# Performance work log

Measured on AMD Instinct MI355X. Metric: run time of the kernel, lower is better.

Reference implementation:

```python
import jax, jax.numpy as jnp
import numpy as np

D_MODEL = 1024
NUM_HEADS = 16
HEAD_DIM = D_MODEL // NUM_HEADS


def setup_inputs() -> dict:
    key = jax.random.key(0)
    ks = jax.random.split(key, 9)
    B, S = 2, 2048
    scale = 1.0 / np.sqrt(D_MODEL)
    inp = {
        "x": jax.random.normal(ks[0], (B, S, D_MODEL), dtype=jnp.float32),
        "Wq": jax.random.normal(ks[1], (D_MODEL, D_MODEL), dtype=jnp.float32) * scale,
        "bq": jnp.zeros((D_MODEL,), dtype=jnp.float32),
        "Wk": jax.random.normal(ks[2], (D_MODEL, D_MODEL), dtype=jnp.float32) * scale,
        "bk": jnp.zeros((D_MODEL,), dtype=jnp.float32),
        "Wv": jax.random.normal(ks[3], (D_MODEL, D_MODEL), dtype=jnp.float32) * scale,
        "bv": jnp.zeros((D_MODEL,), dtype=jnp.float32),
        "Wo": jax.random.normal(ks[4], (D_MODEL, D_MODEL), dtype=jnp.float32) * scale,
        "bo": jnpp_zeros(D_MODEL) if False else jnp.zeros((D_MODEL,), dtype=jnp.float32),
    }
    return inp


def reference(x, Wq, bq, Wk, bk, Wv, bv, Wo, bo):
    B, S, _ = x.shape
    # projections (torch Linear: y = x @ W.T + b; here W stored as [in, out])
    q = x @ Wq + bq  # [B,S,D]
    k = x @ Wk + bk
    v = x @ Wv + bv
    # split heads -> [B,H,S,hd]
    def split(t):
        return t.reshape(B, S, NUM_HEADS, HEAD_DIM).transpose(0, 2, 1, 3)
    q, k, v = split(q), split(k), split(v)
    scale = 1.0 / jnp.sqrt(jnp.asarray(HEAD_DIM, dtype=x.dtype))
    scores = jnp.einsum("bhqd,bhkd->bhqk", q, k) * scale  # [B,H,S,S]
    probs = jax.nn.softmax(scores, axis=-1)
    out = jnp.einsum("bhqk,bhkd->bhqd", probs, v)  # [B,H,S,hd]
    out = out.transpose(0, 2, 1, 3).reshape(B, S, D_MODEL)
    return out @ Wo + bo  # dropout is identity in eval mode
```

## Files before the change

kernel.cpp:

```cpp
#include <hip/hip_runtime.h>

#define D_MODEL 1024
#define NHEADS  16
#define HDIM    64
#define BATCH   2
#define SEQ     2048
#define M_TOK   (BATCH * SEQ)

typedef unsigned short u16;
typedef unsigned int   u32;
typedef __attribute__((ext_vector_type(8))) short  short8;
typedef __attribute__((ext_vector_type(4))) float  floatx4;
typedef __attribute__((ext_vector_type(2))) u32    u32x2;

#define GLOBAL_AS __attribute__((address_space(1)))
#define LDS_AS    __attribute__((address_space(3)))

static __device__ __forceinline__ void gload_lds16(const u16* g, u16* l) {
    __builtin_amdgcn_global_load_lds((const GLOBAL_AS u32*)g, (LDS_AS u32*)l, 16, 0, 0);
}

static __device__ __forceinline__ u16 f2bf(float f) {
    union { float f; u32 i; } v; v.f = f;
    u32 x = v.i;
    return (u16)((x + 0x7fffu + ((x >> 16) & 1u)) >> 16);
}

static __device__ __forceinline__ u32 cvtpk(float a, float b) {
    u32 r;
    asm("v_cvt_pk_bf16_f32 %0, %1, %2" : "=v"(r) : "v"(a), "v"(b));
    return r;
}

static __device__ __forceinline__ short8 ld8_cvt(const float* __restrict__ p) {
    float4 f0 = *(const float4*)(p);
    float4 f1 = *(const float4*)(p + 4);
    short8 r;
    r[0] = (short)f2bf(f0.x); r[1] = (short)f2bf(f0.y);
    r[2] = (short)f2bf(f0.z); r[3] = (short)f2bf(f0.w);
    r[4] = (short)f2bf(f1.x); r[5] = (short)f2bf(f1.y);
    r[6] = (short)f2bf(f1.z); r[7] = (short)f2bf(f1.w);
    return r;
}

__global__ __launch_bounds__(256) void zerofill_k(float* __restrict__ out, int n) {
    int i = blockIdx.x * 256 + threadIdx.x;
    if (i < n) out[i] = 0.f;
}

__global__ __launch_bounds__(1024) void prep_k(const float* __restrict__ x,
                                               const float* __restrict__ W0,
                                               const float* __restrict__ W1,
                                               const float* __restrict__ W2,
                                               const float* __restrict__ W3,
                                               u16* __restrict__ WtBase,
                                               u16* __restrict__ Xb) {
    int z = blockIdx.z;
    if (z == 4) {
        int blk = blockIdx.y * 32 + blockIdx.x;
        int t   = threadIdx.y * 32 + threadIdx.x;
        size_t i0 = ((size_t)blk * 1024 + t) * 4;
        float4 f = *(const float4*)(x + i0);
        u32 lo = (u32)f2bf(f.x) | ((u32)f2bf(f.y) << 16);
        u32 hi = (u32)f2bf(f.z) | ((u32)f2bf(f.w) << 16);
        *(u32*)(Xb + i0)     = lo;
        *(u32*)(Xb + i0 + 2) = hi;
        return;
    }
    const float* W = (z == 0) ? W0 : (z == 1) ? W1 : (z == 2) ? W2 : W3;
    u16* Wt = WtBase + (size_t)z * 1024 * 1024;
    __shared__ u16 tile[32][33];
    int tx = threadIdx.x, ty = threadIdx.y;
    int bx = blockIdx.x * 32, by = blockIdx.y * 32;
    tile[ty][tx] = f2bf(W[(size_t)(by + ty) * 1024 + bx + tx]);
    __syncthreads();
    Wt[(size_t)(bx + ty) * 1024 + by + tx] = tile[tx][ty];
}

template <int MODE, int OUTF32, int MI>
static __device__ __forceinline__ void gemm_core(u16* __restrict__ smem,
                                                 const u16* __restrict__ A,
                                                 const u16* __restrict__ Bt,
                                                 const float* __restrict__ bias,
                                                 float scale,
                                                 void* __restrict__ C,
                                                 int m0, int n0) {
    u16* As = smem;
    u16* Bs = smem + MI * 32 * 32;
    int tid  = threadIdx.x;
    int wave = tid >> 6, lane = tid & 63;
    int quad = lane >> 4, l15 = lane & 15;
    int wm = (wave & 1) * (MI * 16);
    int wn = (wave >> 1) * 64;

    floatx4 acc[MI][4] = {};

    for (int k0 = 0; k0 < 1024; k0 += 32) {
#pragma unroll
        for (int t = 0; t < MI / 2; ++t) {
            int a = t * 256 + tid;
            gload_lds16(A + (size_t)(m0 + (a >> 2)) * 1024 + k0 + (a & 3) * 8, As + (size_t)a * 8);
        }
#pragma unroll
        for (int t = 0; t < 2; ++t) {
            int cb = t * 256 + tid;
            gload_lds16(Bt + (size_t)(n0 + (cb >> 2)) * 1024 + k0 + (cb & 3) * 8, Bs + (size_t)cb * 8);
        }
        __syncthreads();

        short8 af[MI], bfr[4];
#pragma unroll
        for (int i = 0; i < MI; ++i)
            af[i] = *(const short8*)(As + (wm + i * 16 + l15) * 32 + quad * 8);
#pragma unroll
        for (int j = 0; j < 4; ++j)
            bfr[j] = *(const short8*)(Bs + (wn + j * 16 + l15) * 32 + quad * 8);
#pragma unroll
        for (int i = 0; i < MI; ++i)
#pragma unroll
            for (int j = 0; j < 4; ++j)
                acc[i][j] = __builtin_amdgcn_mfma_f32_16x16x32_bf16(af[i], bfr[j], acc[i][j], 0, 0, 0);
        __syncthreads();
    }

    if constexpr (MODE == 2) {
        u16* T = smem;
        int bb = m0 >> 11;
#pragma unroll
        for (int p = 0; p < 2; ++p) {
            if (p) __syncthreads();
            if ((wave >> 1) == p) {
#pragma unroll
                for (int j = 0; j < 4; ++j) {
                    int dcol = j * 16 + l15;
                    float bv = bias[n0 + p * 64 + dcol];
#pragma unroll
                    for (int i = 0; i < MI; ++i) {
#pragma unroll
                        for (int rr = 0; rr < 2; ++rr) {
                            int srow = wm + i * 16 + quad * 4 + rr * 2;
                            u16 lo = f2bf((acc[i][j][rr * 2]     + bv) * scale);
                            u16 hi = f2bf((acc[i][j][rr * 2 + 1] + bv) * scale);
                            *(u32*)(T + dcol * 136 + srow) = (u32)lo | ((u32)hi << 16);
                        }
                    }
                }
            }
            __syncthreads();
            int d  = tid >> 2;
            int sc = (tid & 3) * 32;
            int col = n0 + p * 64 + d;
            int h = col >> 6, dd = col & 63;
            int s0 = (m0 & 2047) + sc;
            size_t gbase = (((size_t)bb * NHEADS + h) * HDIM + dd) * SEQ + s0;
#pragma unroll
            for (int c = 0; c < 4; ++c)
                *(short8*)((u16*)C + gbase + c * 8) = *(const short8*)(T + d * 136 + sc + c * 8);
        }
        return;
    }

#pragma unroll
    for (int j = 0; j < 4; ++j) {
        int col = n0 + wn + j * 16 + l15;
        float bv = bias[col];
#pragma unroll
        for (int i = 0; i < MI; ++i) {
#pragma unroll
            for (int r = 0; r < 4; ++r) {
                int row = m0 + wm + i * 16 + quad * 4 + r;
                float v = (acc[i][j][r] + bv) * scale;
                size_t idx;
                if (MODE == 0) {
                    idx = (size_t)row * 1024 + col;
                } else {
                    int b = row >> 11, s = row & 2047;
                    int h = col >> 6,  d = col & 63;
                    idx = (((size_t)b * NHEADS + h) * SEQ + s) * HDIM + d;
                }
                if constexpr (OUTF32) ((float*)C)[idx] = v;
                else                  ((u16*)C)[idx] = f2bf(v);
            }
        }
    }
}

__global__ __launch_bounds__(256, 3) void gemm_qkv(const u16* __restrict__ X,
                                                   const u16* __restrict__ WtBase,
                                                   const float* __restrict__ bq,
                                                   const float* __restrict__ bk,
                                                   const float* __restrict__ bv,
                                                   u16* __restrict__ OutBase) {
    __shared__ __align__(16) u16 smem[8704];
    int z = blockIdx.z;
    const u16* Bt     = WtBase + (size_t)z * 1024 * 1024;
    const float* bias = (z == 0) ? bq : (z == 1) ? bk : bv;
    u16* C            = OutBase + (size_t)z * (size_t)M_TOK * 1024;
    if (z == 2)
        gemm_core<2, 0, 4>(smem, X, Bt, bias, 1.0f, C, blockIdx.y * 128, blockIdx.x * 128);
    else if (z == 0)
        gemm_core<1, 0, 4>(smem, X, Bt, bias, 0.18033688011112042f , C,
                           blockIdx.y * 128, blockIdx.x * 128);
    else
        gemm_core<1, 0, 4>(smem, X, Bt, bias, 1.0f, C, blockIdx.y * 128, blockIdx.x * 128);
}

__global__ __launch_bounds__(256, 2) void gemm_out(const u16* __restrict__ A,
                                                   const u16* __restrict__ Bt,
                                                   const float* __restrict__ bias,
                                                   float* __restrict__ C) {
    __shared__ __align__(16) u16 smem[6144];
    gemm_core<0, 1, 2>(smem, A, Bt, bias, 1.0f, C, blockIdx.y * 64, blockIdx.x * 128);
}

#define PST2 40
__global__ __launch_bounds__(512, 3) void attn_k(const u16* __restrict__ Q,
                                                 const u16* __restrict__ K,
                                                 const u16* __restrict__ Vt_g,
                                                 u16* __restrict__ O) {
    __shared__ __align__(16) u16 Vt[2][64 * 128];
    __shared__ __align__(16) u16 Kt[2][128 * 64];
    __shared__ __align__(16) u16 Pl[8][16 * PST2];

    int tid  = threadIdx.x;
    int wave = tid >> 6, lane = tid & 63;
    int quad = lane >> 4, l15 = lane & 15;
    int bh = blockIdx.y;
    int b = bh >> 4, h = bh & 15;
    const u16* Qb = Q    + (size_t)bh * SEQ * HDIM;
    const u16* Kb = K    + (size_t)bh * SEQ * HDIM;
    const u16* Vb = Vt_g + (size_t)bh * HDIM * SEQ;
    int q0 = blockIdx.x * 128 + wave * 16;

    short8 qf0 = *(const short8*)(Qb + (size_t)(q0 + l15) * 64 + quad * 8);
    short8 qf1 = *(const short8*)(Qb + (size_t)(q0 + l15) * 64 + 32 + quad * 8);

    short8 onesf;
#pragma unroll
    for (int i = 0; i < 8; ++i) onesf[i] = (short)0x3F80;

    floatx4 o[4] = {};
    floatx4 o_sum = {};

    {
#pragma unroll
        for (int rnd = 0; rnd < 2; ++rnd) {
            int g = rnd * 512 + tid;
            int vrow = g >> 4, vc = g & 15;
            gload_lds16(Vb + (size_t)vrow * SEQ + (vc ^ (vrow & 15)) * 8,
                        Vt[0] + (size_t)g * 8);
            int krow = g >> 3, kc = g & 7;
            gload_lds16(Kb + (size_t)krow * 64 + (kc ^ (krow & 7)) * 8,
                        Kt[0] + (size_t)g * 8);
        }
    }

    for (int it = 0; it < SEQ / 128; ++it) {
        int kv0 = it * 128;
        __syncthreads();

        if (it + 1 < SEQ / 128) {
            u16* vdst = Vt[(it + 1) & 1];
            u16* kdst = Kt[(it + 1) & 1];
#pragma unroll
            for (int rnd = 0; rnd < 2; ++rnd) {
                int g = rnd * 512 + tid;
                int vrow = g >> 4, vc = g & 15;
                gload_lds16(Vb + (size_t)vrow * SEQ + kv0 + 128 + (vc ^ (vrow & 15)) * 8,
                            vdst + (size_t)g * 8);
                int krow = g >> 3, kc = g & 7;
                gload_lds16(Kb + (size_t)(kv0 + 128 + krow) * 64 + (kc ^ (krow & 7)) * 8,
                            kdst + (size_t)g * 8);
            }
        }

        const u16* kb = Kt[it & 1];
        floatx4 s[8];
        __builtin_amdgcn_s_setprio(1);
#pragma unroll
        for (int j = 0; j < 8; ++j) {
            int row = j * 16 + l15;
            const u16* kr = kb + (size_t)row * 64;
            short8 k0 = *(const short8*)(kr + ((quad ^ (l15 & 7)) * 8));
            short8 k1 = *(const short8*)(kr + (((quad + 4) ^ (l15 & 7)) * 8));
            floatx4 a = {};
            a = __builtin_amdgcn_mfma_f32_16x16x32_bf16(k0, qf0, a, 0, 0, 0);
            a = __builtin_amdgcn_mfma_f32_16x16x32_bf16(k1, qf1, a, 0, 0, 0);
            s[j] = a;
        }
        __builtin_amdgcn_s_setprio(0);

        const u16* vb = Vt[it & 1];
#pragma unroll
        for (int kh = 0; kh < 4; ++kh) {
#pragma unroll
            for (int t = 0; t < 2; ++t) {
                int j = kh * 2 + t;
                float p0 = exp2f(s[j][0]), p1 = exp2f(s[j][1]);
                float p2 = exp2f(s[j][2]), p3 = exp2f(s[j][3]);
                u32 w0 = cvtpk(p0, p1), w1 = cvtpk(p2, p3);
                *(u32x2*)(&Pl[wave][l15 * PST2 + t * 16 + quad * 4]) = (u32x2){w0, w1};
            }
            short8 pf = *(const short8*)(&Pl[wave][l15 * PST2 + quad * 8]);
            __builtin_amdgcn_s_setprio(1);
#pragma unroll
            for (int dj = 0; dj < 4; ++dj) {
                int row = dj * 16 + l15;
                int cg  = kh * 4 + quad;
                short8 vf = *(const short8*)(&vb[(row * 16 + (cg ^ l15)) * 8]);
                o[dj] = __builtin_amdgcn_mfma_f32_16x16x32_bf16(pf, vf, o[dj], 0, 0, 0);
            }
            o_sum = __builtin_amdgcn_mfma_f32_16x16x32_bf16(pf, onesf, o_sum, 0, 0, 0);
            __builtin_amdgcn_s_setprio(0);
        }
    }

#pragma unroll
    for (int r = 0; r < 4; ++r) {
        float invq = 1.f / o_sum[r];
        int srow = q0 + quad * 4 + r;
        size_t base = ((size_t)b * SEQ + srow) * D_MODEL + h * HDIM;
#pragma unroll
        for (int dj = 0; dj < 4; ++dj)
            O[base + dj * 16 + l15] = f2bf(o[dj][r] * invq);
    }
}

extern "C" void kernel_launch(void* const* d_in, const int* in_sizes, int n_in,
                              void* d_out, int out_size, void* d_ws, size_t ws_size,
                              hipStream_t stream) {
    const float* x  = (const float*)d_in[0];
    const float* Wq = (const float*)d_in[1];
    const float* bq = (const float*)d_in[2];
    const float* Wk = (const float*)d_in[3];
    const float* bk = (const float*)d_in[4];
    const float* Wv = (const float*)d_in[5];
    const float* bv = (const float*)d_in[6];
    const float* Wo = (const float*)d_in[7];
    const float* bo = (const float*)d_in[8];
    float* out = (float*)d_out;

    char* ws = (char*)d_ws;
    const size_t WSZ = (size_t)1024 * 1024 * sizeof(u16);
    const size_t QSZ = (size_t)M_TOK * 1024 * sizeof(u16);
    const size_t NEED = 4 * WSZ + 4 * QSZ;

    if (ws_size < NEED) {
        zerofill_k<<<dim3((out_size + 255) / 256), 256, 0, stream>>>(out, out_size);
        return;
    }

    u16* wtq = (u16*)(ws);
    u16* wto = (u16*)(ws + 3 * WSZ);
    u16* Qw  = (u16*)(ws + 4 * WSZ);
    u16* Kw  = (u16*)(ws + 4 * WSZ + QSZ);
    u16* Vw  = (u16*)(ws + 4 * WSZ + 2 * QSZ);
    u16* Xb  = (u16*)(ws + 4 * WSZ + 3 * QSZ);
    u16* Aw  = Xb;

    prep_k<<<dim3(32, 32, 5), dim3(32, 32), 0, stream>>>(x, Wq, Wk, Wv, Wo, wtq, Xb);

    gemm_qkv<<<dim3(8, 32, 3), 256, 0, stream>>>(Xb, wtq, bq, bk, bv, Qw);
    attn_k<<<dim3(SEQ / 128, BATCH * NHEADS), 512, 0, stream>>>(Qw, Kw, Vw, Aw);
    gemm_out<<<dim3(8, 64), 256, 0, stream>>>(Aw, wto, bo, out);
}
```

Before: 203.1 us.

## Shrink attention tiles to 64 queries/64 keys and vectorize prep kernel

The attention kernel moves from 512-thread blocks with 128-query, 128-key tiles to 256-thread blocks with 64-query, 64-key tiles. It adjusts the LDS swizzle for the narrower V tile and doubles the grid, aiming for more resident blocks and less LDS per block. The trade-off is that each K/V tile is now reused by fewer query rows, so global traffic and barrier count go up. The prep kernel now uses 256 threads with vectorized float loads and 16-byte bf16 stores for both the x conversion and the weight transpose.

```diff
diff --git a/kernel.cpp b/kernel.cpp
--- a/kernel.cpp
+++ b/kernel.cpp
@@ -48,33 +48,44 @@
     if (i < n) out[i] = 0.f;
 }
 
-__global__ __launch_bounds__(1024) void prep_k(const float* __restrict__ x,
-                                               const float* __restrict__ W0,
-                                               const float* __restrict__ W1,
-                                               const float* __restrict__ W2,
-                                               const float* __restrict__ W3,
-                                               u16* __restrict__ WtBase,
-                                               u16* __restrict__ Xb) {
+__global__ __launch_bounds__(256) void prep_k(const float* __restrict__ x,
+                                              const float* __restrict__ W0,
+                                              const float* __restrict__ W1,
+                                              const float* __restrict__ W2,
+                                              const float* __restrict__ W3,
+                                              u16* __restrict__ WtBase,
+                                              u16* __restrict__ Xb) {
     int z = blockIdx.z;
+    int t = threadIdx.x;
     if (z == 4) {
         int blk = blockIdx.y * 32 + blockIdx.x;
-        int t   = threadIdx.y * 32 + threadIdx.x;
-        size_t i0 = ((size_t)blk * 1024 + t) * 4;
-        float4 f = *(const float4*)(x + i0);
+        size_t i0 = ((size_t)blk * 256 + t) * 16;
+        short8 v0 = ld8_cvt(x + i0);
+        short8 v1 = ld8_cvt(x + i0 + 8);
+        *(short8*)(Xb + i0)     = v0;
+        *(short8*)(Xb + i0 + 8) = v1;
+        return;
+    }
+    const float* W = (z == 0) ? W0 : (z == 1) ? W1 : (z == 2) ? W2 : W3;
+    u16* Wt = WtBase + (size_t)z * 1024 * 1024;
+    __shared__ u16 T[32][34];
+    int bx = blockIdx.x * 32, by = blockIdx.y * 32;
+    {
+        int r = t >> 3, c4 = t & 7;
+        float4 f = *(const float4*)(W + (size_t)(by + r) * 1024 + bx + c4 * 4);
         u32 lo = (u32)f2bf(f.x) | ((u32)f2bf(f.y) << 16);
         u32 hi = (u32)f2bf(f.z) | ((u32)f2bf(f.w) << 16);
-        *(u32*)(Xb + i0)     = lo;
-        *(u32*)(Xb + i0 + 2) = hi;
-        return;
-    }
-    const float* W = (z == 0) ? W0 : (z == 1) ? W1 : (z == 2) ? W2 : W3;
-    u16* Wt = WtBase + (size_t)z * 1024 * 1024;
-    __shared__ u16 tile[32][33];
-    int tx = threadIdx.x, ty = threadIdx.y;
-    int bx = blockIdx.x * 32, by = blockIdx.y * 32;
-    tile[ty][tx] = f2bf(W[(size_t)(by + ty) * 1024 + bx + tx]);
+        *(u32*)(&T[r][c4 * 4])     = lo;
+        *(u32*)(&T[r][c4 * 4 + 2]) = hi;
+    }
     __syncthreads();
-    Wt[(size_t)(bx + ty) * 1024 + by + tx] = tile[tx][ty];
+    if (t < 128) {
+        int n = t >> 2, seg = t & 3;
+        short8 v;
+#pragma unroll
+        for (int i = 0; i < 8; ++i) v[i] = (short)T[seg * 8 + i][n];
+        *(short8*)(Wt + (size_t)(bx + n) * 1024 + by + seg * 8) = v;
+    }
 }
 
 template <int MODE, int OUTF32, int MI>
@@ -214,13 +225,13 @@
 }
 
 #define PST2 40
-__global__ __launch_bounds__(512, 3) void attn_k(const u16* __restrict__ Q,
+__global__ __launch_bounds__(256, 4) void attn_k(const u16* __restrict__ Q,
                                                  const u16* __restrict__ K,
                                                  const u16* __restrict__ Vt_g,
                                                  u16* __restrict__ O) {
-    __shared__ __align__(16) u16 Vt[2][64 * 128];
-    __shared__ __align__(16) u16 Kt[2][128 * 64];
-    __shared__ __align__(16) u16 Pl[8][16 * PST2];
+    __shared__ __align__(16) u16 Vt[2][64 * 64];
+    __shared__ __align__(16) u16 Kt[2][64 * 64];
+    __shared__ __align__(16) u16 Pl[4][16 * PST2];
 
     int tid  = threadIdx.x;
     int wave = tid >> 6, lane = tid & 63;
@@ -230,7 +241,7 @@
     const u16* Qb = Q    + (size_t)bh * SEQ * HDIM;
     const u16* Kb = K    + (size_t)bh * SEQ * HDIM;
     const u16* Vb = Vt_g + (size_t)bh * HDIM * SEQ;
-    int q0 = blockIdx.x * 128 + wave * 16;
+    int q0 = blockIdx.x * 64 + wave * 16;
 
     short8 qf0 = *(const short8*)(Qb + (size_t)(q0 + l15) * 64 + quad * 8);
     short8 qf1 = *(const short8*)(Qb + (size_t)(q0 + l15) * 64 + 32 + quad * 8);
@@ -245,40 +256,38 @@
     {
 #pragma unroll
         for (int rnd = 0; rnd < 2; ++rnd) {
-            int g = rnd * 512 + tid;
-            int vrow = g >> 4, vc = g & 15;
-            gload_lds16(Vb + (size_t)vrow * SEQ + (vc ^ (vrow & 15)) * 8,
+            int g = rnd * 256 + tid;
+            int row = g >> 3, c = g & 7;
+            gload_lds16(Vb + (size_t)row * SEQ + (c ^ (row & 7)) * 8,
                         Vt[0] + (size_t)g * 8);
-            int krow = g >> 3, kc = g & 7;
-            gload_lds16(Kb + (size_t)krow * 64 + (kc ^ (krow & 7)) * 8,
+            gload_lds16(Kb + (size_t)row * 64 + (c ^ (row & 7)) * 8,
                         Kt[0] + (size_t)g * 8);
         }
     }
 
-    for (int it = 0; it < SEQ / 128; ++it) {
-        int kv0 = it * 128;
+    for (int it = 0; it < SEQ / 64; ++it) {
+        int kv0 = it * 64;
         __syncthreads();
 
-        if (it + 1 < SEQ / 128) {
+        if (it + 1 < SEQ / 64) {
             u16* vdst = Vt[(it + 1) & 1];
             u16* kdst = Kt[(it + 1) & 1];
 #pragma unroll
             for (int rnd = 0; rnd < 2; ++rnd) {
-                int g = rnd * 512 + tid;
-                int vrow = g >> 4, vc = g & 15;
-                gload_lds16(Vb + (size_t)vrow * SEQ + kv0 + 128 + (vc ^ (vrow & 15)) * 8,
+                int g = rnd * 256 + tid;
+                int row = g >> 3, c = g & 7;
+                gload_lds16(Vb + (size_t)row * SEQ + kv0 + 64 + (c ^ (row & 7)) * 8,
                             vdst + (size_t)g * 8);
-                int krow = g >> 3, kc = g & 7;
-                gload_lds16(Kb + (size_t)(kv0 + 128 + krow) * 64 + (kc ^ (krow & 7)) * 8,
+                gload_lds16(Kb + (size_t)(kv0 + 64 + row) * 64 + (c ^ (row & 7)) * 8,
                             kdst + (size_t)g * 8);
             }
         }
 
         const u16* kb = Kt[it & 1];
-        floatx4 s[8];
+        floatx4 s[4];
         __builtin_amdgcn_s_setprio(1);
 #pragma unroll
-        for (int j = 0; j < 8; ++j) {
+        for (int j = 0; j < 4; ++j) {
             int row = j * 16 + l15;
             const u16* kr = kb + (size_t)row * 64;
             short8 k0 = *(const short8*)(kr + ((quad ^ (l15 & 7)) * 8));
@@ -292,7 +301,7 @@
 
         const u16* vb = Vt[it & 1];
 #pragma unroll
-        for (int kh = 0; kh < 4; ++kh) {
+        for (int kh = 0; kh < 2; ++kh) {
 #pragma unroll
             for (int t = 0; t < 2; ++t) {
                 int j = kh * 2 + t;
@@ -305,9 +314,9 @@
             __builtin_amdgcn_s_setprio(1);
 #pragma unroll
             for (int dj = 0; dj < 4; ++dj) {
-                int row = dj * 16 + l15;
-                int cg  = kh * 4 + quad;
-                short8 vf = *(const short8*)(&vb[(row * 16 + (cg ^ l15)) * 8]);
+                int drow = dj * 16 + l15;
+                short8 vf = *(const short8*)(&vb[((size_t)drow * 8 +
+                                                  ((kh * 4 + quad) ^ (l15 & 7))) * 8]);
                 o[dj] = __builtin_amdgcn_mfma_f32_16x16x32_bf16(pf, vf, o[dj], 0, 0, 0);
             }
             o_sum = __builtin_amdgcn_mfma_f32_16x16x32_bf16(pf, onesf, o_sum, 0, 0, 0);
@@ -358,9 +367,9 @@
     u16* Xb  = (u16*)(ws + 4 * WSZ + 3 * QSZ);
     u16* Aw  = Xb;
 
-    prep_k<<<dim3(32, 32, 5), dim3(32, 32), 0, stream>>>(x, Wq, Wk, Wv, Wo, wtq, Xb);
+    prep_k<<<dim3(32, 32, 5), 256, 0, stream>>>(x, Wq, Wk, Wv, Wo, wtq, Xb);
 
     gemm_qkv<<<dim3(8, 32, 3), 256, 0, stream>>>(Xb, wtq, bq, bk, bv, Qw);
-    attn_k<<<dim3(SEQ / 128, BATCH * NHEADS), 512, 0, stream>>>(Qw, Kw, Vw, Aw);
+    attn_k<<<dim3(SEQ / 64, BATCH * NHEADS), 256, 0, stream>>>(Qw, Kw, Vw, Aw);
     gemm_out<<<dim3(8, 64), 256, 0, stream>>>(Aw, wto, bo, out);
 }
```

Result: no change. 205.3 us (+1.1%).

## Double GEMM K-tile to 64 with XOR-swizzled LDS and vectorize prep kernel

Applied to the files above, without the earlier changes.

The GEMM core now stages 64-wide K slices per iteration instead of 32. This halves the number of barrier pairs per tile, and an XOR swizzle on the LDS layout avoids bank conflicts on the 128-byte rows. The prep kernel is rewritten to 256 threads using float4 loads and 16-byte stores, for both the x conversion and the weight transpose. LDS per block doubles, which may reduce occupancy for gemm_qkv under its launch bound of 3.

```diff
diff --git a/kernel.cpp b/kernel.cpp
--- a/kernel.cpp
+++ b/kernel.cpp
@@ -48,33 +48,44 @@
     if (i < n) out[i] = 0.f;
 }
 
-__global__ __launch_bounds__(1024) void prep_k(const float* __restrict__ x,
-                                               const float* __restrict__ W0,
-                                               const float* __restrict__ W1,
-                                               const float* __restrict__ W2,
-                                               const float* __restrict__ W3,
-                                               u16* __restrict__ WtBase,
-                                               u16* __restrict__ Xb) {
+__global__ __launch_bounds__(256) void prep_k(const float* __restrict__ x,
+                                              const float* __restrict__ W0,
+                                              const float* __restrict__ W1,
+                                              const float* __restrict__ W2,
+                                              const float* __restrict__ W3,
+                                              u16* __restrict__ WtBase,
+                                              u16* __restrict__ Xb) {
     int z = blockIdx.z;
+    int t = threadIdx.x;
     if (z == 4) {
         int blk = blockIdx.y * 32 + blockIdx.x;
-        int t   = threadIdx.y * 32 + threadIdx.x;
-        size_t i0 = ((size_t)blk * 1024 + t) * 4;
-        float4 f = *(const float4*)(x + i0);
+        size_t i0 = ((size_t)blk * 256 + t) * 16;
+        short8 v0 = ld8_cvt(x + i0);
+        short8 v1 = ld8_cvt(x + i0 + 8);
+        *(short8*)(Xb + i0)     = v0;
+        *(short8*)(Xb + i0 + 8) = v1;
+        return;
+    }
+    const float* W = (z == 0) ? W0 : (z == 1) ? W1 : (z == 2) ? W2 : W3;
+    u16* Wt = WtBase + (size_t)z * 1024 * 1024;
+    __shared__ u16 T[32][34];
+    int bx = blockIdx.x * 32, by = blockIdx.y * 32;
+    {
+        int r = t >> 3, c4 = t & 7;
+        float4 f = *(const float4*)(W + (size_t)(by + r) * 1024 + bx + c4 * 4);
         u32 lo = (u32)f2bf(f.x) | ((u32)f2bf(f.y) << 16);
         u32 hi = (u32)f2bf(f.z) | ((u32)f2bf(f.w) << 16);
-        *(u32*)(Xb + i0)     = lo;
-        *(u32*)(Xb + i0 + 2) = hi;
-        return;
-    }
-    const float* W = (z == 0) ? W0 : (z == 1) ? W1 : (z == 2) ? W2 : W3;
-    u16* Wt = WtBase + (size_t)z * 1024 * 1024;
-    __shared__ u16 tile[32][33];
-    int tx = threadIdx.x, ty = threadIdx.y;
-    int bx = blockIdx.x * 32, by = blockIdx.y * 32;
-    tile[ty][tx] = f2bf(W[(size_t)(by + ty) * 1024 + bx + tx]);
+        *(u32*)(&T[r][c4 * 4])     = lo;
+        *(u32*)(&T[r][c4 * 4 + 2]) = hi;
+    }
     __syncthreads();
-    Wt[(size_t)(bx + ty) * 1024 + by + tx] = tile[tx][ty];
+    if (t < 128) {
+        int n = t >> 2, seg = t & 3;
+        short8 v;
+#pragma unroll
+        for (int i = 0; i < 8; ++i) v[i] = (short)T[seg * 8 + i][n];
+        *(short8*)(Wt + (size_t)(bx + n) * 1024 + by + seg * 8) = v;
+    }
 }
 
 template <int MODE, int OUTF32, int MI>
@@ -86,7 +97,7 @@
                                                  void* __restrict__ C,
                                                  int m0, int n0) {
     u16* As = smem;
-    u16* Bs = smem + MI * 32 * 32;
+    u16* Bs = smem + MI * 32 * 64;
     int tid  = threadIdx.x;
     int wave = tid >> 6, lane = tid & 63;
     int quad = lane >> 4, l15 = lane & 15;
@@ -95,31 +106,39 @@
 
     floatx4 acc[MI][4] = {};
 
-    for (int k0 = 0; k0 < 1024; k0 += 32) {
-#pragma unroll
-        for (int t = 0; t < MI / 2; ++t) {
+    for (int k0 = 0; k0 < 1024; k0 += 64) {
+#pragma unroll
+        for (int t = 0; t < MI; ++t) {
             int a = t * 256 + tid;
-            gload_lds16(A + (size_t)(m0 + (a >> 2)) * 1024 + k0 + (a & 3) * 8, As + (size_t)a * 8);
-        }
-#pragma unroll
-        for (int t = 0; t < 2; ++t) {
-            int cb = t * 256 + tid;
-            gload_lds16(Bt + (size_t)(n0 + (cb >> 2)) * 1024 + k0 + (cb & 3) * 8, Bs + (size_t)cb * 8);
+            int row = a >> 3, c = a & 7;
+            gload_lds16(A + (size_t)(m0 + row) * 1024 + k0 + ((c ^ (row & 7)) * 8),
+                        As + (size_t)a * 8);
+        }
+#pragma unroll
+        for (int t = 0; t < 4; ++t) {
+            int a = t * 256 + tid;
+            int row = a >> 3, c = a & 7;
+            gload_lds16(Bt + (size_t)(n0 + row) * 1024 + k0 + ((c ^ (row & 7)) * 8),
+                        Bs + (size_t)a * 8);
         }
         __syncthreads();
 
-        short8 af[MI], bfr[4];
-#pragma unroll
-        for (int i = 0; i < MI; ++i)
-            af[i] = *(const short8*)(As + (wm + i * 16 + l15) * 32 + quad * 8);
-#pragma unroll
-        for (int j = 0; j < 4; ++j)
-            bfr[j] = *(const short8*)(Bs + (wn + j * 16 + l15) * 32 + quad * 8);
-#pragma unroll
-        for (int i = 0; i < MI; ++i)
+#pragma unroll
+        for (int h = 0; h < 2; ++h) {
+            int g = ((h * 4 + quad) ^ (l15 & 7)) * 8;
+            short8 af[MI], bfr[4];
+#pragma unroll
+            for (int i = 0; i < MI; ++i)
+                af[i] = *(const short8*)(As + (wm + i * 16 + l15) * 64 + g);
 #pragma unroll
             for (int j = 0; j < 4; ++j)
-                acc[i][j] = __builtin_amdgcn_mfma_f32_16x16x32_bf16(af[i], bfr[j], acc[i][j], 0, 0, 0);
+                bfr[j] = *(const short8*)(Bs + (wn + j * 16 + l15) * 64 + g);
+#pragma unroll
+            for (int i = 0; i < MI; ++i)
+#pragma unroll
+                for (int j = 0; j < 4; ++j)
+                    acc[i][j] = __builtin_amdgcn_mfma_f32_16x16x32_bf16(af[i], bfr[j], acc[i][j], 0, 0, 0);
+        }
         __syncthreads();
     }
 
@@ -191,7 +210,7 @@
                                                    const float* __restrict__ bk,
                                                    const float* __restrict__ bv,
                                                    u16* __restrict__ OutBase) {
-    __shared__ __align__(16) u16 smem[8704];
+    __shared__ __align__(16) u16 smem[16384];
     int z = blockIdx.z;
     const u16* Bt     = WtBase + (size_t)z * 1024 * 1024;
     const float* bias = (z == 0) ? bq : (z == 1) ? bk : bv;
@@ -209,7 +228,7 @@
                                                    const u16* __restrict__ Bt,
                                                    const float* __restrict__ bias,
                                                    float* __restrict__ C) {
-    __shared__ __align__(16) u16 smem[6144];
+    __shared__ __align__(16) u16 smem[12288];
     gemm_core<0, 1, 2>(smem, A, Bt, bias, 1.0f, C, blockIdx.y * 64, blockIdx.x * 128);
 }
 
@@ -358,7 +377,7 @@
     u16* Xb  = (u16*)(ws + 4 * WSZ + 3 * QSZ);
     u16* Aw  = Xb;
 
-    prep_k<<<dim3(32, 32, 5), dim3(32, 32), 0, stream>>>(x, Wq, Wk, Wv, Wo, wtq, Xb);
+    prep_k<<<dim3(32, 32, 5), 256, 0, stream>>>(x, Wq, Wk, Wv, Wo, wtq, Xb);
 
     gemm_qkv<<<dim3(8, 32, 3), 256, 0, stream>>>(Xb, wtq, bq, bk, bv, Qw);
     attn_k<<<dim3(SEQ / 128, BATCH * NHEADS), 512, 0, stream>>>(Qw, Kw, Vw, Aw);
```

New measurement: 196.6 us. 1.03x faster.
